# Kernel optimization log

Measured on AMD Instinct MI355X. Metric: run time of the kernel, lower is better.

Reference implementation:

```python
import jax, jax.numpy as jnp
import numpy as np
from itertools import combinations

B, F, C, MAX_ORDER = 4096, 32, 128, 3


def setup_inputs() -> dict:
    key = jax.random.key(0)
    ks = jax.random.split(key, 1 + MAX_ORDER)
    x = jax.random.normal(ks[0], (B, F), dtype=jnp.float32)
    # Exact combinatorial index lists, matching get_index_lists (all k-subsets, lexicographic)
    idx = [jnp.asarray(np.array(list(combinations(range(F), o)), dtype=np.int32))
           for o in range(1, MAX_ORDER + 1)]
    # Per-order Dense kernels [n_combos, num_classes] (glorot-ish scale), no bias (use_bias=False)
    Ws = [jax.random.normal(ks[i + 1], (idx[i].shape[0], C), dtype=jnp.float32)
          * (2.0 / (idx[i].shape[0] + C)) ** 0.5 for i in range(MAX_ORDER)]
    bias = jnp.zeros((1, C), dtype=jnp.float32)  # Zeros initializer
    return {"x": x, "bias": bias,
            "W1": Ws[0], "W2": Ws[1], "W3": Ws[2],
            "idx1": idx[0], "idx2": idx[1], "idx3": idx[2]}


def reference(x, bias, W1, W2, W3, idx1, idx2, idx3):
    # combine(): out = tile(bias) + sum_i Dense_i( prod over feature-subset of order i )
    out = jnp.broadcast_to(bias, (x.shape[0], bias.shape[1]))
    for idx, W in ((idx1, W1), (idx2, W2), (idx3, W3)):
        # x[:, idx]: [B, n_combos, order] gather; product over subset axis -> [B, n_combos]
        prods = jnp.prod(x[:, idx], axis=2)
        out = out + prods @ W  # [B, num_classes]
    return out
```

## Files before the change

kernel.cpp:

```cpp
#include <hip/hip_runtime.h>
#include <hip/hip_bf16.h>

constexpr int B_   = 4096;
constexpr int C_   = 128;
constexpr int K1   = 32;
constexpr int K2   = 496;
constexpr int K3   = 4960;
constexpr int KTOT = K1 + K2 + K3;
constexpr int KPAD = 5632;

constexpr int NCHUNK = KPAD / 16;
constexpr int WCH    = NCHUNK / 4;

typedef __attribute__((ext_vector_type(8)))  short bf16x8;
typedef __attribute__((ext_vector_type(16))) float f32x16;

constexpr size_t WS_WT = 0;

struct Sched { short a[KPAD]; short b[KPAD]; short c[KPAD]; };
constexpr Sched make_sched() {
    Sched s{}; int k = 0;
    for (int i = 0; i < 32; ++i) { s.a[k] = i; s.b[k] = 32; s.c[k] = 32; ++k; }
    for (int i = 0; i < 32; ++i)
        for (int j = i + 1; j < 32; ++j) { s.a[k] = i; s.b[k] = j; s.c[k] = 32; ++k; }
    for (int i = 0; i < 32; ++i)
        for (int j = i + 1; j < 32; ++j)
            for (int l = j + 1; l < 32; ++l) { s.a[k] = i; s.b[k] = j; s.c[k] = l; ++k; }
    for (; k < KPAD; ++k) { s.a[k] = 32; s.b[k] = 32; s.c[k] = 32; }
    return s;
}
constexpr Sched SCH = make_sched();

template<int K>
__device__ __forceinline__ float prodK(const float (&xv)[33]) {
    return xv[SCH.a[K]] * xv[SCH.b[K]] * xv[SCH.c[K]];
}

template<int K0, int J>
__device__ __forceinline__ void prods8(const float (&xv)[33], bool hi, float (&q)[8]) {
    if constexpr (J < 8) {
        q[J] = hi ? prodK<K0 + 8 + J>(xv) : prodK<K0 + J>(xv);
        prods8<K0, J + 1>(xv, hi, q);
    }
}

template<int WV, int CH>
__device__ __forceinline__ void run_chunks(const float (&xv)[33], bool hi, int lane, int ct,
                                           const ushort* __restrict__ Wb, f32x16& acc) {
    if constexpr (CH < WCH) {
        constexpr int G  = WV * WCH + CH;
        constexpr int K0 = G * 16;
        bf16x8 b0 = *(const bf16x8*)(Wb + ((size_t)(G * 4 + ct) * 64 + lane) * 8);
        float q[8];
        prods8<K0, 0>(xv, hi, q);
        union { ushort us[8]; bf16x8 v; } af;
        #pragma unroll
        for (int j = 0; j < 8; ++j) {
            __hip_bfloat16 h = __float2bfloat16(q[j]);
            af.us[j] = *reinterpret_cast<ushort*>(&h);
        }
        acc = __builtin_amdgcn_mfma_f32_32x32x16_bf16(af.v, b0, acc, 0, 0, 0);
        run_chunks<WV, CH + 1>(xv, hi, lane, ct, Wb, acc);
    }
}

__global__ __launch_bounds__(256)
void prep_wt(const float* __restrict__ W1,
             const float* __restrict__ W2,
             const float* __restrict__ W3,
             ushort* __restrict__ Wb)
{
    __shared__ ushort tile[16 * 130];
    const int gc = blockIdx.x, t = threadIdx.x;
    const int k0 = gc * 16;
    #pragma unroll
    for (int p = 0; p < 2; ++p) {
        int e  = p * 256 + t;
        int kk = e >> 5, cq = e & 31;
        int k  = k0 + kk;
        float4 v = {0.f, 0.f, 0.f, 0.f};
        if (k < K1)           v = ((const float4*)W1)[k * 32 + cq];
        else if (k < K1 + K2) v = ((const float4*)W2)[(k - K1) * 32 + cq];
        else if (k < KTOT)    v = ((const float4*)W3)[(k - K1 - K2) * 32 + cq];
        union { ushort u[4]; uint2 d; } o;
        __hip_bfloat16 h0 = __float2bfloat16(v.x); o.u[0] = *(ushort*)&h0;
        __hip_bfloat16 h1 = __float2bfloat16(v.y); o.u[1] = *(ushort*)&h1;
        __hip_bfloat16 h2 = __float2bfloat16(v.z); o.u[2] = *(ushort*)&h2;
        __hip_bfloat16 h3 = __float2bfloat16(v.w); o.u[3] = *(ushort*)&h3;
        *(uint2*)&tile[kk * 130 + cq * 4] = o.d;
    }
    __syncthreads();
    {
        int ct = t >> 6, lane = t & 63, n = lane & 31, kg = lane >> 5;
        union { ushort us[8]; uint4 d; } o;
        #pragma unroll
        for (int j = 0; j < 8; ++j) o.us[j] = tile[(kg * 8 + j) * 130 + ct * 32 + n];
        *(uint4*)&Wb[((size_t)(gc * 4 + ct) * 64 + lane) * 8] = o.d;
    }
}

__global__ __launch_bounds__(256, 2)
void poly_mfma(const float* __restrict__ x,
               const ushort* __restrict__ Wb,
               const float* __restrict__ bias,
               float* __restrict__ out)
{
    __shared__ float red[4][32 * 33];

    const int t    = threadIdx.x;
    const int lane = t & 63;
    const int w    = t >> 6;
    const int m    = lane & 31;
    const bool hi  = lane >= 32;
    const int row0 = blockIdx.x * 32;
    const int ct   = blockIdx.y;

    float xv[33];
    {
        const float4* xrow = (const float4*)(x + (size_t)(row0 + m) * 32);
        #pragma unroll
        for (int qv = 0; qv < 8; ++qv) {
            float4 v = xrow[qv];
            xv[qv * 4 + 0] = v.x; xv[qv * 4 + 1] = v.y;
            xv[qv * 4 + 2] = v.z; xv[qv * 4 + 3] = v.w;
        }
        xv[32] = 1.0f;
    }

    f32x16 acc;
    #pragma unroll
    for (int i = 0; i < 16; ++i) acc[i] = 0.f;

    switch (w) {
        case 0:  run_chunks<0, 0>(xv, hi, lane, ct, Wb, acc); break;
        case 1:  run_chunks<1, 0>(xv, hi, lane, ct, Wb, acc); break;
        case 2:  run_chunks<2, 0>(xv, hi, lane, ct, Wb, acc); break;
        default: run_chunks<3, 0>(xv, hi, lane, ct, Wb, acc); break;
    }

    const int kg = hi ? 1 : 0;
    #pragma unroll
    for (int e = 0; e < 16; ++e) {
        int r = (e & 3) + 8 * (e >> 2) + 4 * kg;
        red[w][r * 33 + m] = acc[e];
    }
    __syncthreads();

    {
        int r  = t >> 3;
        int c0 = (t & 7) * 4;
        float4 b = *(const float4*)&bias[ct * 32 + c0];
        float s[4] = {b.x, b.y, b.z, b.w};
        #pragma unroll
        for (int wv = 0; wv < 4; ++wv)
            #pragma unroll
            for (int j = 0; j < 4; ++j)
                s[j] += red[wv][r * 33 + c0 + j];
        float4 o = {s[0], s[1], s[2], s[3]};
        *(float4*)&out[(size_t)(row0 + r) * C_ + ct * 32 + c0] = o;
    }
}

extern "C" void kernel_launch(void* const* d_in, const int* in_sizes, int n_in,
                              void* d_out, int out_size, void* d_ws, size_t ws_size,
                              hipStream_t stream)
{
    const float* x    = (const float*)d_in[0];
    const float* bias = (const float*)d_in[1];
    const float* W1   = (const float*)d_in[2];
    const float* W2   = (const float*)d_in[3];
    const float* W3   = (const float*)d_in[4];
    float* out = (float*)d_out;

    ushort* Wb = (ushort*)((char*)d_ws + WS_WT);

    prep_wt<<<KPAD / 16, 256, 0, stream>>>(W1, W2, W3, Wb);

    dim3 grid(B_ / 32, C_ / 32);
    poly_mfma<<<grid, 256, 0, stream>>>(x, Wb, bias, out);
}
```

Before: 82.31 us.

## Process 64 rows per block with 2-way K split and drop K padding

Each block now covers 64 rows: two wave pairs take separate 32-row tiles, and the K dimension is split in two halves instead of four quarters. This halves the number of blocks and the cross-wave reduction work. The K range is no longer padded to 5632 and stops at the exact 5488 terms, which removes the zero-product MFMAs and the padded weight rows. The catch is that each wave runs a longer serial MFMA chain, roughly 172 chunks instead of 88, so there is less parallelism per row tile.

```diff
diff --git a/kernel.cpp b/kernel.cpp
--- a/kernel.cpp
+++ b/kernel.cpp
@@ -7,17 +7,15 @@
 constexpr int K2   = 496;
 constexpr int K3   = 4960;
 constexpr int KTOT = K1 + K2 + K3;
-constexpr int KPAD = 5632;
-
-constexpr int NCHUNK = KPAD / 16;
-constexpr int WCH    = NCHUNK / 4;
+constexpr int NCH  = KTOT / 16;
+constexpr int CHSPLIT = 172;
 
 typedef __attribute__((ext_vector_type(8)))  short bf16x8;
 typedef __attribute__((ext_vector_type(16))) float f32x16;
 
 constexpr size_t WS_WT = 0;
 
-struct Sched { short a[KPAD]; short b[KPAD]; short c[KPAD]; };
+struct Sched { short a[KTOT]; short b[KTOT]; short c[KTOT]; };
 constexpr Sched make_sched() {
     Sched s{}; int k = 0;
     for (int i = 0; i < 32; ++i) { s.a[k] = i; s.b[k] = 32; s.c[k] = 32; ++k; }
@@ -26,7 +24,6 @@
     for (int i = 0; i < 32; ++i)
         for (int j = i + 1; j < 32; ++j)
             for (int l = j + 1; l < 32; ++l) { s.a[k] = i; s.b[k] = j; s.c[k] = l; ++k; }
-    for (; k < KPAD; ++k) { s.a[k] = 32; s.b[k] = 32; s.c[k] = 32; }
     return s;
 }
 constexpr Sched SCH = make_sched();
@@ -44,13 +41,12 @@
     }
 }
 
-template<int WV, int CH>
+template<int CH, int CHEND>
 __device__ __forceinline__ void run_chunks(const float (&xv)[33], bool hi, int lane, int ct,
                                            const ushort* __restrict__ Wb, f32x16& acc) {
-    if constexpr (CH < WCH) {
-        constexpr int G  = WV * WCH + CH;
-        constexpr int K0 = G * 16;
-        bf16x8 b0 = *(const bf16x8*)(Wb + ((size_t)(G * 4 + ct) * 64 + lane) * 8);
+    if constexpr (CH < CHEND) {
+        constexpr int K0 = CH * 16;
+        bf16x8 b0 = *(const bf16x8*)(Wb + ((size_t)(CH * 4 + ct) * 64 + lane) * 8);
         float q[8];
         prods8<K0, 0>(xv, hi, q);
         union { ushort us[8]; bf16x8 v; } af;
@@ -60,7 +56,7 @@
             af.us[j] = *reinterpret_cast<ushort*>(&h);
         }
         acc = __builtin_amdgcn_mfma_f32_32x32x16_bf16(af.v, b0, acc, 0, 0, 0);
-        run_chunks<WV, CH + 1>(xv, hi, lane, ct, Wb, acc);
+        run_chunks<CH + 1, CHEND>(xv, hi, lane, ct, Wb, acc);
     }
 }
 
@@ -110,14 +106,15 @@
     const int t    = threadIdx.x;
     const int lane = t & 63;
     const int w    = t >> 6;
+    const int rt   = w & 1;
     const int m    = lane & 31;
     const bool hi  = lane >= 32;
-    const int row0 = blockIdx.x * 32;
+    const int row0 = blockIdx.x * 64;
     const int ct   = blockIdx.y;
 
     float xv[33];
     {
-        const float4* xrow = (const float4*)(x + (size_t)(row0 + m) * 32);
+        const float4* xrow = (const float4*)(x + (size_t)(row0 + rt * 32 + m) * 32);
         #pragma unroll
         for (int qv = 0; qv < 8; ++qv) {
             float4 v = xrow[qv];
@@ -131,12 +128,8 @@
     #pragma unroll
     for (int i = 0; i < 16; ++i) acc[i] = 0.f;
 
-    switch (w) {
-        case 0:  run_chunks<0, 0>(xv, hi, lane, ct, Wb, acc); break;
-        case 1:  run_chunks<1, 0>(xv, hi, lane, ct, Wb, acc); break;
-        case 2:  run_chunks<2, 0>(xv, hi, lane, ct, Wb, acc); break;
-        default: run_chunks<3, 0>(xv, hi, lane, ct, Wb, acc); break;
-    }
+    if (w < 2) run_chunks<0, CHSPLIT>(xv, hi, lane, ct, Wb, acc);
+    else       run_chunks<CHSPLIT, NCH>(xv, hi, lane, ct, Wb, acc);
 
     const int kg = hi ? 1 : 0;
     #pragma unroll
@@ -147,17 +140,20 @@
     __syncthreads();
 
     {
-        int r  = t >> 3;
-        int c0 = (t & 7) * 4;
-        float4 b = *(const float4*)&bias[ct * 32 + c0];
-        float s[4] = {b.x, b.y, b.z, b.w};
+        int r  = t >> 2;
+        int c0 = (t & 3) * 8;
+        int rtile = r >> 5, rr = r & 31;
+        float s[8];
         #pragma unroll
-        for (int wv = 0; wv < 4; ++wv)
-            #pragma unroll
-            for (int j = 0; j < 4; ++j)
-                s[j] += red[wv][r * 33 + c0 + j];
-        float4 o = {s[0], s[1], s[2], s[3]};
-        *(float4*)&out[(size_t)(row0 + r) * C_ + ct * 32 + c0] = o;
+        for (int j = 0; j < 8; ++j) {
+            float b = bias[ct * 32 + c0 + j];
+            s[j] = b + red[rtile][rr * 33 + c0 + j] + red[rtile + 2][rr * 33 + c0 + j];
+        }
+        float4 o0 = {s[0], s[1], s[2], s[3]};
+        float4 o1 = {s[4], s[5], s[6], s[7]};
+        float* op = &out[(size_t)(row0 + r) * C_ + ct * 32 + c0];
+        *(float4*)op       = o0;
+        *(float4*)(op + 4) = o1;
     }
 }
 
@@ -174,8 +170,8 @@
 
     ushort* Wb = (ushort*)((char*)d_ws + WS_WT);
 
-    prep_wt<<<KPAD / 16, 256, 0, stream>>>(W1, W2, W3, Wb);
+    prep_wt<<<NCH, 256, 0, stream>>>(W1, W2, W3, Wb);
 
-    dim3 grid(B_ / 32, C_ / 32);
+    dim3 grid(B_ / 64, C_ / 32);
     poly_mfma<<<grid, 256, 0, stream>>>(x, Wb, bias, out);
 }
```

Result: slower. 101.3 us (+23.0%).
